# Kernel optimization log

Measured on AMD Instinct MI355X. Metric: run time of the kernel, lower is better.

Reference implementation:

```python
import jax, jax.numpy as jnp
import numpy as np

# ---- static configuration (mirrors ConvolutionConfig) ----
B_IMG, C_IN, H, W = 8, 16, 32, 32
C_OUT = 64
KH, KW = 5, 5          # receptive_field
SH, SW = 2, 2          # stride
PH, PW = 2, 2          # padding
N_BITS = 6             # n_inputs_per_node
HIDDEN = [36, 6, 1]    # 6^2, 6^1, 6^0 (tree_depth=2)
INPUT_SIZE = C_IN * KH * KW  # 400
OH = (H + 2 * PH - KH) // SH + 1  # 16
OW = (W + 2 * PW - KW) // SW + 1  # 16


def setup_inputs() -> dict:
    key = jax.random.key(0)
    ks = jax.random.split(key, 7)
    x = jax.random.uniform(ks[0], (B_IMG, C_IN, H, W), dtype=jnp.float32)
    # per-tree random input mappings (6 inputs per LUT node)
    idx0 = jax.random.randint(ks[1], (C_OUT, HIDDEN[0], N_BITS), 0, INPUT_SIZE)
    idx1 = jax.random.randint(ks[2], (C_OUT, HIDDEN[1], N_BITS), 0, HIDDEN[0])
    idx2 = jax.random.randint(ks[3], (C_OUT, HIDDEN[2], N_BITS), 0, HIDDEN[1])
    # raw LUT tables (64 entries), passed through sigmoid in forward
    table0 = jax.random.normal(ks[4], (C_OUT, HIDDEN[0], 64), dtype=jnp.float32)
    table1 = jax.random.normal(ks[5], (C_OUT, HIDDEN[1], 64), dtype=jnp.float32)
    table2 = jax.random.normal(ks[6], (C_OUT, HIDDEN[2], 64), dtype=jnp.float32)
    return {"x": x, "idx0": idx0, "table0": table0, "idx1": idx1,
            "table1": table1, "idx2": idx2, "table2": table2}


def _unfold(x):
    """torch nn.Unfold equivalent -> rows of [B*L, C*KH*KW], c slowest."""
    xp = jnp.pad(x, ((0, 0), (0, 0), (PH, PH), (PW, PW)))
    ri = (jnp.arange(OH) * SH)[:, None] + jnp.arange(KH)[None, :]  # [OH,KH]
    ci = (jnp.arange(OW) * SW)[:, None] + jnp.arange(KW)[None, :]  # [OW,KW]
    # [B, C, OH, OW, KH, KW]
    p = xp[:, :, ri[:, None, :, None], ci[None, :, None, :]]
    p = jnp.transpose(p, (0, 2, 3, 1, 4, 5))  # [B, OH, OW, C, KH, KW]
    return p.reshape(B_IMG * OH * OW, INPUT_SIZE)


def _lut_nodes(g, table):
    """Differentiable LUT node (multilinear interpolation over 2^6 table).
    g: [B, T, N, 6] probabilistic bits in [0,1]; table: [T, N, 64].
    Output: [B, T, N] = sum_a sigmoid(table)[a] * prod_i (g_i if bit_i(a) else 1-g_i).
    Computed by sequential bit contraction to avoid a [B,T,N,64] product tensor.
    """
    T, N = table.shape[0], table.shape[1]
    f = jnp.stack([1.0 - g, g], axis=-1)  # [B,T,N,6,2]
    w = jax.nn.sigmoid(table)             # [T,N,64]
    # contract most-significant bit first
    acc = jnp.einsum('tnkr,btnk->btnr', w.reshape(T, N, 2, 32), f[..., 0, :])
    for b in range(1, N_BITS):
        acc = jnp.einsum('btnkr,btnk->btnr',
                         acc.reshape(acc.shape[0], T, N, 2, -1), f[..., b, :])
    return acc[..., 0]  # [B,T,N]


def reference(x, idx0, table0, idx1, table1, idx2, table2):
    p = _unfold(x)                       # [BP, 400], BP = B*OH*OW
    tind = jnp.arange(C_OUT)[:, None, None]
    # first layer (chunked in torch; mathematically one big gathered layer)
    g0 = p[:, idx0]                      # [BP, C_OUT, 36, 6]
    h0 = _lut_nodes(g0, table0)          # [BP, C_OUT, 36]
    # tree layer 1: 36 -> 6 per tree
    g1 = h0[:, tind, idx1]               # [BP, C_OUT, 6, 6]
    h1 = _lut_nodes(g1, table1)          # [BP, C_OUT, 6]
    # tree layer 2: 6 -> 1 per tree
    g2 = h1[:, tind, idx2]               # [BP, C_OUT, 1, 6]
    h2 = _lut_nodes(g2, table2)[..., 0]  # [BP, C_OUT]
    out = h2.reshape(B_IMG, OH * OW, C_OUT)
    out = jnp.transpose(out, (0, 2, 1)).reshape(B_IMG, C_OUT, OH, OW)
    return out
```

## Files before the change

kernel.cpp:

```cpp
#include <hip/hip_runtime.h>

#define B_IMG 8
#define C_IN  16
#define COUT  64
#define H0    36
#define H1    6
#define NB    6
#define NNODE 43

typedef float f32x2 __attribute__((ext_vector_type(2)));

__device__ __forceinline__ float sigf(float v) { return 1.0f / (1.0f + __expf(-v)); }
__device__ __forceinline__ float4 sig4(float4 a) {
    return make_float4(sigf(a.x), sigf(a.y), sigf(a.z), sigf(a.w));
}

__device__ __forceinline__ float lut_contract_reg(const float4 lo4[8], const float4 dd4[8],
                                                  const float g[NB]) {
    f32x2 v[16];
    const float g0 = g[0];
#pragma unroll
    for (int q = 0; q < 8; ++q) {
        v[2*q+0] = (f32x2){lo4[q].x, lo4[q].y} + (f32x2){dd4[q].x, dd4[q].y} * g0;
        v[2*q+1] = (f32x2){lo4[q].z, lo4[q].w} + (f32x2){dd4[q].z, dd4[q].w} * g0;
    }
#pragma unroll
    for (int i = 1; i < 5; ++i) {
        const int vh = 16 >> i;
        const float gi = g[i];
#pragma unroll
        for (int r = 0; r < vh; ++r)
            v[r] += (v[r + vh] - v[r]) * gi;
    }
    return v[0].x + (v[0].y - v[0].x) * g[5];
}

__device__ __forceinline__ void load_tbl_lds(const float* tb, float4 lo4[8], float4 dd4[8]) {
    const float4* t4 = (const float4*)tb;
#pragma unroll
    for (int q = 0; q < 8; ++q) { lo4[q] = t4[q]; dd4[q] = t4[q + 8]; }
}

__global__ __launch_bounds__(256) void lutone_kernel(
    const float* __restrict__ x,
    const int*   __restrict__ idx0,
    const float* __restrict__ t0,
    const int*   __restrict__ idx1,
    const float* __restrict__ t1,
    const int*   __restrict__ idx2,
    const float* __restrict__ t2,
    float*       __restrict__ out)
{
    __shared__ float tblL[NNODE*64];
    __shared__ float h0s[H0*128];
    __shared__ float h1s[H1*128];
    __shared__ int   metaL[H0*NB*2];
    __shared__ int   idx1L[H1*NB];
    __shared__ int   idx2L[NB];

    const int tid  = threadIdx.x;
    const int w    = tid >> 6;
    const int lane = tid & 63;
    const int b    = blockIdx.x;
    const int t    = b & 63;
    const int img  = (b >> 6) & 7;
    const int half = b >> 9;

    {
        float4* tbl4 = (float4*)tblL;
        for (int e = tid; e < NNODE*8; e += 256) {
            const int node = e >> 3, q = e & 7;
            const float* src = (node < H0)      ? t0 + ((size_t)t*H0 + node)*64
                             : (node < H0+H1)   ? t1 + ((size_t)t*H1 + node - H0)*64
                                                : t2 + (size_t)t*64;
            const float4* s4 = (const float4*)src;
            const float4 lo = sig4(s4[q]);
            const float4 hi = sig4(s4[q + 8]);
            tbl4[node*16 + q]     = lo;
            tbl4[node*16 + 8 + q] = make_float4(hi.x - lo.x, hi.y - lo.y,
                                                hi.z - lo.z, hi.w - lo.w);
        }
    }
    if (tid < H0*NB) {
        const int raw = idx0[(size_t)t*(H0*NB) + tid];
        const int c2  = raw / 25;
        const int rem = raw - 25*c2;
        const int kh  = rem / 5, kw = rem - 5*kh;
        metaL[tid*2 + 0] = c2*1024 + kh*32 + kw - 66;
        metaL[tid*2 + 1] = rem;
    }
    if (tid < H1*NB) idx1L[tid] = idx1[(size_t)t*(H1*NB) + tid];
    if (tid < NB)    idx2L[tid] = idx2[(size_t)t*NB + tid];

    const int* i1base = idx1 + t*(H1*NB);
    unsigned long long umask = 0ull;
#pragma unroll
    for (int j = 0; j < H1*NB; ++j) umask |= 1ull << i1base[j];

    int base[2], vmask[2];
#pragma unroll
    for (int c = 0; c < 2; ++c) {
        const int p  = half*128 + (c << 6) + lane;
        const int oh = p >> 4, ow = p & 15;
        base[c] = img*16384 + oh*64 + ow*2;
        const int hm = 0x1F ^ ((oh == 0) ? 0x03 : 0) ^ ((oh == 15) ? 0x10 : 0);
        const int wm = 0x1F ^ ((ow == 0) ? 0x03 : 0) ^ ((ow == 15) ? 0x10 : 0);
        int vm = 0;
#pragma unroll
        for (int kh = 0; kh < 5; ++kh)
            vm |= ((hm >> kh) & 1) ? (wm << (5*kh)) : 0;
        vmask[c] = vm;
    }

    int myn0=-1, myn1=-1, myn2=-1, myn3=-1, myn4=-1, myn5=-1, myn6=-1, myn7=-1, myn8=-1;
    {
        int cnt = 0;
        for (int n = 0; n < H0; ++n) {
            if (!((umask >> n) & 1ull)) continue;
            const int slot = cnt++;
            if ((slot & 3) != w) continue;
            switch (slot >> 2) {
                case 0: myn0 = n; break;
                case 1: myn1 = n; break;
                case 2: myn2 = n; break;
                case 3: myn3 = n; break;
                case 4: myn4 = n; break;
                case 5: myn5 = n; break;
                case 6: myn6 = n; break;
                case 7: myn7 = n; break;
                default: myn8 = n; break;
            }
        }
    }
    __syncthreads();

#define GATH(dst, C)                                                         \
    _Pragma("unroll")                                                        \
    for (int i = 0; i < NB; ++i) {                                           \
        const bool ok = ((vmask[C] >> rem_[i]) & 1) != 0;                    \
        const float v = x[ok ? (base[C] + off_[i]) : 0];                     \
        dst[i] = ok ? v : 0.0f;                                              \
    }
#define NODE_A(NN)                                                           \
    if ((NN) >= 0) {                                                         \
        const int4* mp = (const int4*)(metaL + (NN)*12);                     \
        const int4 ma = mp[0], mb = mp[1], mc = mp[2];                       \
        const int off_[NB] = {ma.x, ma.z, mb.x, mb.z, mc.x, mc.z};           \
        const int rem_[NB] = {ma.y, ma.w, mb.y, mb.w, mc.y, mc.w};           \
        float gA[NB], gB[NB];                                                \
        GATH(gA, 0)                                                          \
        float4 lo4[8], dd4[8];                                               \
        load_tbl_lds(tblL + (NN)*64, lo4, dd4);                              \
        GATH(gB, 1)                                                          \
        h0s[(NN)*128 + lane]      = lut_contract_reg(lo4, dd4, gA);          \
        h0s[(NN)*128 + 64 + lane] = lut_contract_reg(lo4, dd4, gB);          \
    }
    NODE_A(myn0)
    NODE_A(myn1)
    NODE_A(myn2)
    NODE_A(myn3)
    NODE_A(myn4)
    NODE_A(myn5)
    NODE_A(myn6)
    NODE_A(myn7)
    NODE_A(myn8)
#undef NODE_A
#undef GATH
    __syncthreads();

#pragma unroll
    for (int j = 0; j < 3; ++j) {
        const int u = 3*w + j;
        const int n = u >> 1, c = u & 1;
        float4 lo4[8], dd4[8];
        load_tbl_lds(tblL + (H0 + n)*64, lo4, dd4);
        const int* i1 = idx1L + n*NB;
        const int px = (c << 6) + lane;
        float g[NB];
#pragma unroll
        for (int i = 0; i < NB; ++i) g[i] = h0s[i1[i]*128 + px];
        h1s[n*128 + px] = lut_contract_reg(lo4, dd4, g);
    }
    __syncthreads();

    if (w < 2) {
        float4 lo4[8], dd4[8];
        load_tbl_lds(tblL + (H0 + H1)*64, lo4, dd4);
        const int px = (w << 6) + lane;
        float g[NB];
#pragma unroll
        for (int i = 0; i < NB; ++i) g[i] = h1s[idx2L[i]*128 + px];
        out[((size_t)img*COUT + t)*256 + half*128 + px] = lut_contract_reg(lo4, dd4, g);
    }
}

extern "C" void kernel_launch(void* const* d_in, const int* in_sizes, int n_in,
                              void* d_out, int out_size, void* d_ws, size_t ws_size,
                              hipStream_t stream) {
    const float* x      = (const float*)d_in[0];
    const int*   idx0   = (const int*)  d_in[1];
    const float* table0 = (const float*)d_in[2];
    const int*   idx1   = (const int*)  d_in[3];
    const float* table1 = (const float*)d_in[4];
    const int*   idx2   = (const int*)  d_in[5];
    const float* table2 = (const float*)d_in[6];
    float* out = (float*)d_out;

    lutone_kernel<<<COUT * B_IMG * 2, 256, 0, stream>>>(
        x, idx0, table0, idx1, table1, idx2, table2, out);
}
```

Baseline: 23.90 us.

## Process full image per block, store layer-0 outputs as fp16

Each block now covers all 256 output pixels of one (tree, image) pair instead of half, which halves the grid. Table setup work and sigmoid evaluation are each done once per tree and image rather than twice, and every node's table registers are reused across 4 pixel groups. The intermediate h0 values are kept in LDS as fp16 to fit the larger tile. Layers 1 and 2 now use all 256 threads. The cost is fewer blocks (512) for occupancy, extra register pressure, and a small loss of precision in h0.

```diff
diff --git a/kernel.cpp b/kernel.cpp
--- a/kernel.cpp
+++ b/kernel.cpp
@@ -1,4 +1,5 @@
 #include <hip/hip_runtime.h>
+#include <hip/hip_fp16.h>
 
 #define B_IMG 8
 #define C_IN  16
@@ -9,36 +10,35 @@
 #define NNODE 43
 
 typedef float f32x2 __attribute__((ext_vector_type(2)));
+typedef float f32x4 __attribute__((ext_vector_type(4)));
 
 __device__ __forceinline__ float sigf(float v) { return 1.0f / (1.0f + __expf(-v)); }
 __device__ __forceinline__ float4 sig4(float4 a) {
     return make_float4(sigf(a.x), sigf(a.y), sigf(a.z), sigf(a.w));
 }
 
-__device__ __forceinline__ float lut_contract_reg(const float4 lo4[8], const float4 dd4[8],
-                                                  const float g[NB]) {
-    f32x2 v[16];
+__device__ __forceinline__ float lut_tree(const f32x4 lo[8], const f32x4 dd[8],
+                                          const float g[NB]) {
+    f32x4 v[8];
     const float g0 = g[0];
 #pragma unroll
-    for (int q = 0; q < 8; ++q) {
-        v[2*q+0] = (f32x2){lo4[q].x, lo4[q].y} + (f32x2){dd4[q].x, dd4[q].y} * g0;
-        v[2*q+1] = (f32x2){lo4[q].z, lo4[q].w} + (f32x2){dd4[q].z, dd4[q].w} * g0;
-    }
-#pragma unroll
-    for (int i = 1; i < 5; ++i) {
-        const int vh = 16 >> i;
-        const float gi = g[i];
-#pragma unroll
-        for (int r = 0; r < vh; ++r)
-            v[r] += (v[r + vh] - v[r]) * gi;
-    }
-    return v[0].x + (v[0].y - v[0].x) * g[5];
-}
-
-__device__ __forceinline__ void load_tbl_lds(const float* tb, float4 lo4[8], float4 dd4[8]) {
-    const float4* t4 = (const float4*)tb;
-#pragma unroll
-    for (int q = 0; q < 8; ++q) { lo4[q] = t4[q]; dd4[q] = t4[q + 8]; }
+    for (int q = 0; q < 8; ++q) v[q] = lo[q] + dd[q] * g0;
+    const float g1 = g[1], g2 = g[2], g3 = g[3];
+#pragma unroll
+    for (int q = 0; q < 4; ++q) v[q] += (v[q + 4] - v[q]) * g1;
+#pragma unroll
+    for (int q = 0; q < 2; ++q) v[q] += (v[q + 2] - v[q]) * g2;
+    v[0] += (v[1] - v[0]) * g3;
+    f32x2 a = {v[0].x, v[0].y};
+    const f32x2 b = {v[0].z, v[0].w};
+    a += (b - a) * g[4];
+    return a.x + (a.y - a.x) * g[5];
+}
+
+__device__ __forceinline__ void load_tbl(const float* tb, f32x4 lo[8], f32x4 dd[8]) {
+    const f32x4* t4 = (const f32x4*)tb;
+#pragma unroll
+    for (int q = 0; q < 8; ++q) { lo[q] = t4[q]; dd[q] = t4[q + 8]; }
 }
 
 __global__ __launch_bounds__(256) void lutone_kernel(
@@ -51,20 +51,18 @@
     const float* __restrict__ t2,
     float*       __restrict__ out)
 {
-    __shared__ float tblL[NNODE*64];
-    __shared__ float h0s[H0*128];
-    __shared__ float h1s[H1*128];
-    __shared__ int   metaL[H0*NB*2];
-    __shared__ int   idx1L[H1*NB];
-    __shared__ int   idx2L[NB];
+    __shared__ float  tblL[NNODE*64];
+    __shared__ __half h0s[H0*256];
+    __shared__ float  h1s[H1*256];
+    __shared__ int    metaL[H0*NB*2];
+    __shared__ int    idx1L[H1*NB];
+    __shared__ int    idx2L[NB];
 
     const int tid  = threadIdx.x;
     const int w    = tid >> 6;
     const int lane = tid & 63;
-    const int b    = blockIdx.x;
-    const int t    = b & 63;
-    const int img  = (b >> 6) & 7;
-    const int half = b >> 9;
+    const int t    = blockIdx.x & 63;
+    const int img  = blockIdx.x >> 6;
 
     {
         float4* tbl4 = (float4*)tblL;
@@ -97,10 +95,10 @@
 #pragma unroll
     for (int j = 0; j < H1*NB; ++j) umask |= 1ull << i1base[j];
 
-    int base[2], vmask[2];
-#pragma unroll
-    for (int c = 0; c < 2; ++c) {
-        const int p  = half*128 + (c << 6) + lane;
+    int base[4], vmask[4];
+#pragma unroll
+    for (int c = 0; c < 4; ++c) {
+        const int p  = (c << 6) + lane;
         const int oh = p >> 4, ow = p & 15;
         base[c] = img*16384 + oh*64 + ow*2;
         const int hm = 0x1F ^ ((oh == 0) ? 0x03 : 0) ^ ((oh == 15) ? 0x10 : 0);
@@ -134,26 +132,29 @@
     }
     __syncthreads();
 
-#define GATH(dst, C)                                                         \
-    _Pragma("unroll")                                                        \
-    for (int i = 0; i < NB; ++i) {                                           \
-        const bool ok = ((vmask[C] >> rem_[i]) & 1) != 0;                    \
-        const float v = x[ok ? (base[C] + off_[i]) : 0];                     \
-        dst[i] = ok ? v : 0.0f;                                              \
-    }
 #define NODE_A(NN)                                                           \
     if ((NN) >= 0) {                                                         \
         const int4* mp = (const int4*)(metaL + (NN)*12);                     \
         const int4 ma = mp[0], mb = mp[1], mc = mp[2];                       \
         const int off_[NB] = {ma.x, ma.z, mb.x, mb.z, mc.x, mc.z};           \
         const int rem_[NB] = {ma.y, ma.w, mb.y, mb.w, mc.y, mc.w};           \
-        float gA[NB], gB[NB];                                                \
-        GATH(gA, 0)                                                          \
-        float4 lo4[8], dd4[8];                                               \
-        load_tbl_lds(tblL + (NN)*64, lo4, dd4);                              \
-        GATH(gB, 1)                                                          \
-        h0s[(NN)*128 + lane]      = lut_contract_reg(lo4, dd4, gA);          \
-        h0s[(NN)*128 + 64 + lane] = lut_contract_reg(lo4, dd4, gB);          \
+        f32x4 lo[8], dd[8];                                                  \
+        load_tbl(tblL + (NN)*64, lo, dd);                                    \
+        _Pragma("unroll")                                                    \
+        for (int q = 0; q < 8; ++q)                                          \
+            asm volatile("" : "+v"(lo[q]), "+v"(dd[q]));   \
+        _Pragma("unroll")                                                    \
+        for (int c = 0; c < 4; ++c) {                                        \
+            float g[NB];                                                     \
+            _Pragma("unroll")                                                \
+            for (int i = 0; i < NB; ++i) {                                   \
+                const bool ok = ((vmask[c] >> rem_[i]) & 1) != 0;            \
+                const float v = x[ok ? (base[c] + off_[i]) : 0];             \
+                g[i] = ok ? v : 0.0f;                                        \
+            }                                                                \
+            const float r = lut_tree(lo, dd, g);                             \
+            h0s[(NN)*256 + (c << 6) + lane] = __float2half(r);               \
+        }                                                                    \
     }
     NODE_A(myn0)
     NODE_A(myn1)
@@ -165,32 +166,29 @@
     NODE_A(myn7)
     NODE_A(myn8)
 #undef NODE_A
-#undef GATH
     __syncthreads();
 
-#pragma unroll
-    for (int j = 0; j < 3; ++j) {
-        const int u = 3*w + j;
-        const int n = u >> 1, c = u & 1;
-        float4 lo4[8], dd4[8];
-        load_tbl_lds(tblL + (H0 + n)*64, lo4, dd4);
-        const int* i1 = idx1L + n*NB;
-        const int px = (c << 6) + lane;
+    {
+#pragma unroll
+        for (int n = 0; n < H1; ++n) {
+            f32x4 lo[8], dd[8];
+            load_tbl(tblL + (H0 + n)*64, lo, dd);
+            const int* i1 = idx1L + n*NB;
+            float g[NB];
+#pragma unroll
+            for (int i = 0; i < NB; ++i) g[i] = __half2float(h0s[i1[i]*256 + tid]);
+            h1s[n*256 + tid] = lut_tree(lo, dd, g);
+        }
+    }
+    __syncthreads();
+
+    {
+        f32x4 lo[8], dd[8];
+        load_tbl(tblL + (H0 + H1)*64, lo, dd);
         float g[NB];
 #pragma unroll
-        for (int i = 0; i < NB; ++i) g[i] = h0s[i1[i]*128 + px];
-        h1s[n*128 + px] = lut_contract_reg(lo4, dd4, g);
-    }
-    __syncthreads();
-
-    if (w < 2) {
-        float4 lo4[8], dd4[8];
-        load_tbl_lds(tblL + (H0 + H1)*64, lo4, dd4);
-        const int px = (w << 6) + lane;
-        float g[NB];
-#pragma unroll
-        for (int i = 0; i < NB; ++i) g[i] = h1s[idx2L[i]*128 + px];
-        out[((size_t)img*COUT + t)*256 + half*128 + px] = lut_contract_reg(lo4, dd4, g);
+        for (int i = 0; i < NB; ++i) g[i] = h1s[idx2L[i]*256 + tid];
+        out[((size_t)img*COUT + t)*256 + tid] = lut_tree(lo, dd, g);
     }
 }
 
@@ -206,6 +204,6 @@
     const float* table2 = (const float*)d_in[6];
     float* out = (float*)d_out;
 
-    lutone_kernel<<<COUT * B_IMG * 2, 256, 0, stream>>>(
+    lutone_kernel<<<COUT * B_IMG, 256, 0, stream>>>(
         x, idx0, table0, idx1, table1, idx2, table2, out);
 }
```

After: 25.28 us. +5.8%, slower.
